# Kernel optimization log

Measured on AMD Instinct MI355X. Metric: run time of the kernel, lower is better.

## Reference

```python
import jax, jax.numpy as jnp
import numpy as np

B, T, C, H = 8, 1024, 768, 12
HD = C // H  # 64, even for RoPE
ROPE_THETA = 10000.0


def precompute_freqs_cis(dim, end, theta=ROPE_THETA):
    # [end, dim//2, 2] with (cos, sin) in last axis
    freqs = 1.0 / theta ** (jnp.arange(0, dim // 2).astype(jnp.float32) / (dim // 2))
    t = jnp.arange(end)
    f = jnp.outer(t, freqs)
    return jnp.stack([jnp.cos(f), jnp.sin(f)], axis=-1)


def apply_rope(x, fc):
    # x: [B,T,H,hd]; fc: [T,1,hd//2,2] (broadcasts over B and H)
    xr = x.reshape(*x.shape[:-1], -1, 2)
    x_re, x_im = xr[..., 0], xr[..., 1]
    cos, sin = fc[..., 0], fc[..., 1]
    out_re = x_re * cos - x_im * sin
    out_im = x_re * sin + x_im * cos
    return jnp.stack([out_re, out_im], axis=-1).reshape(x.shape)


def setup_inputs() -> dict:
    key = jax.random.key(0)
    k0, k1, k2 = jax.random.split(key, 3)
    x = jax.random.normal(k0, (B, T, C), jnp.float32)
    Wqkv = jax.random.normal(k1, (C, 3 * C), jnp.float32) * 0.02
    bqkv = jnp.zeros((3 * C,), jnp.float32)
    Wproj = jax.random.normal(k2, (C, C), jnp.float32) * 0.02
    bproj = jnp.zeros((C,), jnp.float32)
    mask = jnp.tril(jnp.ones((T, T), jnp.int32))  # causal
    return {"x": x, "Wqkv": Wqkv, "bqkv": bqkv, "Wproj": Wproj, "bproj": bproj, "mask": mask}


def reference(x, Wqkv, bqkv, Wproj, bproj, mask):
    B_, T_, C_ = x.shape
    qkv = (x @ Wqkv + bqkv).reshape(B_, T_, 3, H, HD)
    q, k, v = qkv[:, :, 0], qkv[:, :, 1], qkv[:, :, 2]  # each [B,T,H,hd]
    fc = precompute_freqs_cis(HD, T_)[:, None]  # [T,1,hd//2,2]
    q = apply_rope(q, fc)
    k = apply_rope(k, fc)
    scale = 1.0 / jnp.sqrt(jnp.float32(HD))
    attn = jnp.einsum('bthd,bkhd->bhtk', q, k) * scale  # [B,H,T,T]
    neg = jnp.finfo(attn.dtype).min
    attn = jnp.where(mask[None, None, :, :] == 0, neg, attn)
    attn = jax.nn.softmax(attn, axis=-1)
    out = jnp.einsum('bhtk,bkhd->bthd', attn, v).reshape(B_, T_, C_)
    return out @ Wproj + bproj
```

## Files before the change

kernel.cpp:

```cpp
#include <hip/hip_runtime.h>
#include <cstdint>
#include <cstddef>

#define BB 8
#define TT 1024
#define CC 768
#define NH 12
#define HD 64

using bf16x8 = __attribute__((ext_vector_type(8))) short;
using f32x4  = __attribute__((ext_vector_type(4))) float;

static __device__ __forceinline__ short f2bf(float f) {
    uint32_t u;
    __builtin_memcpy(&u, &f, 4);
    u += 0x7FFFu + ((u >> 16) & 1u);
    return (short)(u >> 16);
}

static __device__ __forceinline__ uint32_t bfpack(float lo, float hi) {
    return (uint32_t)(uint16_t)f2bf(lo) | ((uint32_t)(uint16_t)f2bf(hi) << 16);
}

#define GLOAD_LDS16(gp, lp)                                                        \
    __builtin_amdgcn_global_load_lds(                                              \
        (const __attribute__((address_space(1))) void*)(gp),                       \
        (__attribute__((address_space(3))) void*)(lp), 16, 0, 0)

__global__ void fc_kernel(float2* __restrict__ fc) {
    int idx = blockIdx.x * 256 + threadIdx.x;
    int t = idx >> 5, p = idx & 31;
    float freq = powf(10000.0f, -(float)p / 32.0f);
    float a = (float)t * freq;
    fc[idx] = make_float2(cosf(a), sinf(a));
}

__global__ __launch_bounds__(256)
void cast_kernel(const float* __restrict__ in, short* __restrict__ out) {
    int i = (blockIdx.x * 256 + threadIdx.x) * 8;
    float4 f0 = *(const float4*)(in + i);
    float4 f1 = *(const float4*)(in + i + 4);
    bf16x8 h;
    h[0] = f2bf(f0.x); h[1] = f2bf(f0.y); h[2] = f2bf(f0.z); h[3] = f2bf(f0.w);
    h[4] = f2bf(f1.x); h[5] = f2bf(f1.y); h[6] = f2bf(f1.z); h[7] = f2bf(f1.w);
    *(bf16x8*)(out + i) = h;
}

__global__ __launch_bounds__(256)
void transpose_cast_kernel(const float* __restrict__ in, short* __restrict__ out,
                           int R, int Cdim) {
    __shared__ float tile[32][33];
    int tx = threadIdx.x, ty = threadIdx.y;
    int c0 = blockIdx.x * 32, r0 = blockIdx.y * 32;
#pragma unroll
    for (int i = 0; i < 4; i++)
        tile[ty + 8 * i][tx] = in[(size_t)(r0 + ty + 8 * i) * Cdim + c0 + tx];
    __syncthreads();
#pragma unroll
    for (int i = 0; i < 4; i++)
        out[(size_t)(c0 + ty + 8 * i) * R + r0 + tx] = f2bf(tile[tx][ty + 8 * i]);
}

__global__ __launch_bounds__(256)
void vtrans_kernel(const short* __restrict__ V, short* __restrict__ VT) {
    __shared__ short tl[64][72];
    const int tid = threadIdx.x;
    const int bh = blockIdx.y, t0 = blockIdx.x * 64;
    {
        int r = tid >> 2, cs = (tid & 3) * 16;
        const short* src = V + (size_t)bh * TT * HD + (size_t)(t0 + r) * HD + cs;
        *(bf16x8*)&tl[r][cs]     = *(const bf16x8*)src;
        *(bf16x8*)&tl[r][cs + 8] = *(const bf16x8*)(src + 8);
    }
    __syncthreads();
    {
        int d = tid >> 2, ts = (tid & 3) * 16;
        bf16x8 o0, o1;
#pragma unroll
        for (int e = 0; e < 8; e++) { o0[e] = tl[ts + e][d]; o1[e] = tl[ts + 8 + e][d]; }
        short* dst = VT + (size_t)bh * TT * HD + (size_t)d * TT + t0 + ts;
        *(bf16x8*)dst       = o0;
        *(bf16x8*)(dst + 8) = o1;
    }
}

template <int EPI>
__global__ __launch_bounds__(256)
void gemm_kernel(const short* __restrict__ Agl, const short* __restrict__ BT,
                 const float* __restrict__ bias,
                 short* __restrict__ Qb, short* __restrict__ Kb, short* __restrict__ Vb,
                 const float2* __restrict__ fc, float* __restrict__ out) {
    __shared__ __align__(16) char smem[65536];
    const int tid = threadIdx.x;
    const int lane = tid & 63, wid = tid >> 6;
    const int g = lane >> 4, c = lane & 15;
    const int wm = wid >> 1, wn = wid & 1;

    const int nx = gridDim.x;
    const int bid = blockIdx.y * nx + blockIdx.x;
    const int cpx = (nx * gridDim.y) >> 3;
    const int swz = (bid & 7) * cpx + (bid >> 3);
    const int m0 = (swz / nx) * 128, n0 = (swz % nx) * 128;

    const int sr = lane >> 2;
    const int scol = (((lane & 3) ^ ((sr >> 1) & 3)) << 3);
    const short* Abase = Agl + (size_t)(m0 + wid * 32 + sr) * 768 + scol;
    const short* Bbase = BT  + (size_t)(n0 + wid * 32 + sr) * 768 + scol;

#define A_SLOT(b, kh, q) (smem + (b) * 32768 + (kh) * 8192 + wid * 2048 + (q) * 1024)
#define B_SLOT(b, kh, q) (smem + (b) * 32768 + 16384 + (kh) * 8192 + wid * 2048 + (q) * 1024)
#define STAGE(b, kh, kt)                                                   \
    {                                                                      \
        size_t ko = (size_t)(kt) * 64 + (kh) * 32;                         \
        GLOAD_LDS16(Abase + ko, A_SLOT(b, kh, 0));                         \
        GLOAD_LDS16(Abase + 16 * 768 + ko, A_SLOT(b, kh, 1));              \
        GLOAD_LDS16(Bbase + ko, B_SLOT(b, kh, 0));                         \
        GLOAD_LDS16(Bbase + 16 * 768 + ko, B_SLOT(b, kh, 1));              \
    }

    const f32x4 zero4 = {0.f, 0.f, 0.f, 0.f};
    f32x4 acc[4][4];
#pragma unroll
    for (int i = 0; i < 4; i++)
#pragma unroll
        for (int j = 0; j < 4; j++) acc[i][j] = zero4;

    STAGE(0, 0, 0);
    STAGE(0, 1, 0);
    STAGE(1, 0, 1);
    asm volatile("s_waitcnt vmcnt(8)" ::: "memory");
    __builtin_amdgcn_s_barrier();

    for (int t = 0; t < 12; t++) {
        const int buf = t & 1;
        const int t1 = (t + 1 < 12) ? t + 1 : t - 11;
        const int t2 = (t + 2 < 12) ? t + 2 : t - 10;
#pragma unroll
        for (int kk = 0; kk < 2; kk++) {
            const short* Ab = (const short*)(smem + buf * 32768 + kk * 8192);
            const short* Bb = (const short*)(smem + buf * 32768 + 16384 + kk * 8192);
            bf16x8 af[4], bfr[4];
#pragma unroll
            for (int mi = 0; mi < 4; mi++) {
                int row = wm * 64 + mi * 16 + c;
                af[mi] = *(const bf16x8*)&Ab[row * 32 + ((g ^ ((row >> 1) & 3)) << 3)];
            }
#pragma unroll
            for (int ni = 0; ni < 4; ni++) {
                int row = wn * 64 + ni * 16 + c;
                bfr[ni] = *(const bf16x8*)&Bb[row * 32 + ((g ^ ((row >> 1) & 3)) << 3)];
            }
            if (kk == 0) STAGE(buf ^ 1, 1, t1)
            else         STAGE(buf, 0, t2)
            __builtin_amdgcn_s_barrier();
            __builtin_amdgcn_s_setprio(1);
#pragma unroll
            for (int mi = 0; mi < 4; mi++)
#pragma unroll
                for (int ni = 0; ni < 4; ni++)
                    acc[mi][ni] = __builtin_amdgcn_mfma_f32_16x16x32_bf16(
                        af[mi], bfr[ni], acc[mi][ni], 0, 0, 0);
            __builtin_amdgcn_s_setprio(0);
            asm volatile("s_waitcnt vmcnt(8)" ::: "memory");
            __builtin_amdgcn_s_barrier();
        }
    }

    asm volatile("s_waitcnt vmcnt(0)" ::: "memory");
    __builtin_amdgcn_s_barrier();

    if (EPI == 0) {
        uint32_t* LD = (uint32_t*)smem;
#pragma unroll
        for (int ni = 0; ni < 4; ni++) {
            int nl = wn * 64 + ni * 16 + c;
            int n = n0 + nl;
            float bv = bias[n];
            int part = (n >= 1536) ? 2 : (n >= 768 ? 1 : 0);
            int d = (n - part * 768) & 63;
#pragma unroll
            for (int mi = 0; mi < 4; mi++) {
#pragma unroll
                for (int r = 0; r < 4; r++) {
                    int ml = wm * 64 + mi * 16 + g * 4 + r;
                    float v = acc[mi][ni][r] + bv;
                    float pv = __shfl_xor(v, 1);
                    if (!(c & 1)) {
                        float o0, o1;
                        if (part < 2) {
                            int t = (m0 + ml) & 1023;
                            float2 cs = fc[t * 32 + (d >> 1)];
                            o0 = v * cs.x - pv * cs.y;
                            o1 = v * cs.y + pv * cs.x;
                            if (part == 0) { o0 *= 0.125f; o1 *= 0.125f; }
                        } else { o0 = v; o1 = pv; }
                        LD[ml * 64 + ((nl >> 1) ^ (((ml >> 2) & 3) << 3))] = bfpack(o0, o1);
                    }
                }
            }
        }
        __syncthreads();
#pragma unroll
        for (int p = 0; p < 8; p++) {
            int ml = p * 16 + (tid >> 4);
            int wc = (tid & 15) * 4;
            int4 dat = *(const int4*)&LD[ml * 64 + (wc ^ (((ml >> 2) & 3) << 3))];
            int n = n0 + wc * 2;
            int part = (n >= 1536) ? 2 : (n >= 768 ? 1 : 0);
            int rem = n - part * 768;
            int h = rem >> 6, d = rem & 63;
            int m = m0 + ml, b = m >> 10, t = m & 1023;
            short* dst = (part == 0 ? Qb : part == 1 ? Kb : Vb)
                         + (((size_t)b * NH + h) * TT + t) * HD + d;
            *(int4*)dst = dat;
        }
    } else {
#pragma unroll
        for (int mi = 0; mi < 4; mi++)
#pragma unroll
            for (int ni = 0; ni < 4; ni++) {
                int n = n0 + wn * 64 + ni * 16 + c;
                float bv = bias[n];
#pragma unroll
                for (int r = 0; r < 4; r++) {
                    int m = m0 + wm * 64 + mi * 16 + g * 4 + r;
                    out[(size_t)m * CC + n] = acc[mi][ni][r] + bv;
                }
            }
    }
#undef A_SLOT
#undef B_SLOT
#undef STAGE
}

__global__ __launch_bounds__(256)
void attn_kernel(const short* __restrict__ Qb, const short* __restrict__ Kb,
                 const short* __restrict__ VT, short* __restrict__ Ob) {
    __shared__ uint32_t Pt[4][32][32];
    __shared__ uint32_t ot[128 * 32];
    const int tid = threadIdx.x, lane = tid & 63, wid = tid >> 6;
    const int g = lane >> 4, c = lane & 15;
    const int bh = blockIdx.x, qb = 7 - (int)blockIdx.y;
    const int b = bh / NH, h = bh % NH;
    const short* Qp = Qb + (size_t)bh * TT * HD;
    const short* Kp = Kb + (size_t)bh * TT * HD;
    const short* Vp = VT + (size_t)bh * TT * HD;
    const int q0 = qb * 128 + wid * 32;
    const int sw = (c & 7) << 2;

    bf16x8 qf[2][2];
#pragma unroll
    for (int qs = 0; qs < 2; qs++)
#pragma unroll
        for (int kh = 0; kh < 2; kh++)
            qf[qs][kh] = *(const bf16x8*)(Qp + (size_t)(q0 + qs * 16 + c) * HD + kh * 32 + g * 8);

    const f32x4 zero4 = {0.f, 0.f, 0.f, 0.f};
    f32x4 o[2][4];
#pragma unroll
    for (int qs = 0; qs < 2; qs++)
#pragma unroll
        for (int dt = 0; dt < 4; dt++) o[qs][dt] = zero4;
    float mrun[2] = {-1e30f, -1e30f}, lrun[2] = {0.f, 0.f};

    const int t0max = ((q0 + 31) >> 6) << 6;
    for (int t0 = 0; t0 <= t0max; t0 += 64) {
        f32x4 st[2][4];
#pragma unroll
        for (int nt = 0; nt < 4; nt++) {
            const short* kp = Kp + (size_t)(t0 + nt * 16 + c) * HD + g * 8;
            bf16x8 k0 = *(const bf16x8*)kp;
            bf16x8 k1 = *(const bf16x8*)(kp + 32);
#pragma unroll
            for (int qs = 0; qs < 2; qs++) {
                f32x4 z = zero4;
                z = __builtin_amdgcn_mfma_f32_16x16x32_bf16(k0, qf[qs][0], z, 0, 0, 0);
                z = __builtin_amdgcn_mfma_f32_16x16x32_bf16(k1, qf[qs][1], z, 0, 0, 0);
                st[qs][nt] = z;
            }
        }
        bf16x8 vf[2][4];
#pragma unroll
        for (int blk = 0; blk < 2; blk++)
#pragma unroll
            for (int dt = 0; dt < 4; dt++)
                vf[blk][dt] = *(const bf16x8*)(Vp + (size_t)(dt * 16 + c) * TT + t0 + blk * 32 + g * 8);
        if (t0 + 63 > q0) {
#pragma unroll
            for (int qs = 0; qs < 2; qs++) {
                int q = q0 + qs * 16 + c;
#pragma unroll
                for (int nt = 0; nt < 4; nt++)
#pragma unroll
                    for (int r = 0; r < 4; r++)
                        if (t0 + nt * 16 + g * 4 + r > q) st[qs][nt][r] = -1e30f;
            }
        }
#pragma unroll
        for (int qs = 0; qs < 2; qs++) {
            float mx = st[qs][0][0];
#pragma unroll
            for (int nt = 0; nt < 4; nt++)
#pragma unroll
                for (int r = 0; r < 4; r++) mx = fmaxf(mx, st[qs][nt][r]);
            mx = fmaxf(mx, __shfl_xor(mx, 16));
            mx = fmaxf(mx, __shfl_xor(mx, 32));
            float mnew = fmaxf(mrun[qs], mx);
            float al = __expf(mrun[qs] - mnew);
            mrun[qs] = mnew;
            float sm = 0.f;
#pragma unroll
            for (int nt = 0; nt < 4; nt++)
#pragma unroll
                for (int r = 0; r < 4; r++) {
                    float e = __expf(st[qs][nt][r] - mnew);
                    st[qs][nt][r] = e;
                    sm += e;
                }
            sm += __shfl_xor(sm, 16);
            sm += __shfl_xor(sm, 32);
            lrun[qs] = lrun[qs] * al + sm;
#pragma unroll
            for (int dt = 0; dt < 4; dt++) {
                o[qs][dt][0] *= al; o[qs][dt][1] *= al;
                o[qs][dt][2] *= al; o[qs][dt][3] *= al;
            }
            int row = qs * 16 + c;
#pragma unroll
            for (int nt = 0; nt < 4; nt++) {
                uint32_t w0 = bfpack(st[qs][nt][0], st[qs][nt][1]);
                uint32_t w1 = bfpack(st[qs][nt][2], st[qs][nt][3]);
                int wa = nt * 8 + 2 * g;
                Pt[wid][row][wa ^ sw]       = w0;
                Pt[wid][row][(wa + 1) ^ sw] = w1;
            }
        }
#pragma unroll
        for (int qs = 0; qs < 2; qs++) {
            int row = qs * 16 + c;
#pragma unroll
            for (int blk = 0; blk < 2; blk++) {
                bf16x8 pf = *(const bf16x8*)&Pt[wid][row][(blk * 16 + 4 * g) ^ sw];
#pragma unroll
                for (int dt = 0; dt < 4; dt++)
                    o[qs][dt] = __builtin_amdgcn_mfma_f32_16x16x32_bf16(
                        vf[blk][dt], pf, o[qs][dt], 0, 0, 0);
            }
        }
    }

#pragma unroll
    for (int qs = 0; qs < 2; qs++) {
        float inv = 1.0f / lrun[qs];
        int ql = wid * 32 + qs * 16 + c;
#pragma unroll
        for (int dt = 0; dt < 4; dt++) {
            uint32_t w0 = bfpack(o[qs][dt][0] * inv, o[qs][dt][1] * inv);
            uint32_t w1 = bfpack(o[qs][dt][2] * inv, o[qs][dt][3] * inv);
            int jc0 = dt * 8 + 2 * g;
            int jc1 = jc0 + 1;
            ot[ql * 32 + ((((jc0 >> 2) ^ (c & 7)) << 2) | (jc0 & 3))] = w0;
            ot[ql * 32 + ((((jc1 >> 2) ^ (c & 7)) << 2) | (jc1 & 3))] = w1;
        }
    }
    __syncthreads();
#pragma unroll
    for (int p = 0; p < 4; p++) {
        int q = (tid >> 3) + 32 * p;
        int jb = tid & 7;
        const uint32_t* src = &ot[q * 32 + ((jb ^ (q & 7)) << 2)];
        int4 w = *(const int4*)src;
        *(int4*)(Ob + ((size_t)b * TT + qb * 128 + q) * CC + h * HD + jb * 8) = w;
    }
}

extern "C" void kernel_launch(void* const* d_in, const int* in_sizes, int n_in,
                              void* d_out, int out_size, void* d_ws, size_t ws_size,
                              hipStream_t stream) {
    const float* x     = (const float*)d_in[0];
    const float* Wqkv  = (const float*)d_in[1];
    const float* bqkv  = (const float*)d_in[2];
    const float* Wproj = (const float*)d_in[3];
    const float* bproj = (const float*)d_in[4];

    char* ws = (char*)d_ws;
    short*  WqkvT  = (short*)(ws);
    short*  WprojT = (short*)(ws + 3538944);
    float2* fc     = (float2*)(ws + 3538944 + 1179648);
    short*  Qb     = (short*)(ws + 4980736);
    short*  Kb     = (short*)(ws + 4980736 + 1 * 12582912);
    short*  VOb    = (short*)(ws + 4980736 + 2 * 12582912);
    short*  VbT    = (short*)(ws + 4980736 + 3 * 12582912);
    short*  xb     = VbT;
    float*  out    = (float*)d_out;

    hipLaunchKernelGGL(fc_kernel, dim3(128), dim3(256), 0, stream, fc);
    hipLaunchKernelGGL(transpose_cast_kernel, dim3(72, 24), dim3(32, 8), 0, stream,
                       Wqkv, WqkvT, 768, 2304);
    hipLaunchKernelGGL(transpose_cast_kernel, dim3(24, 24), dim3(32, 8), 0, stream,
                       Wproj, WprojT, 768, 768);
    hipLaunchKernelGGL(cast_kernel, dim3(3072), dim3(256), 0, stream, x, xb);
    hipLaunchKernelGGL((gemm_kernel<0>), dim3(18, 64), dim3(256), 0, stream,
                       xb, WqkvT, bqkv, Qb, Kb, VOb, fc, (float*)nullptr);
    hipLaunchKernelGGL(vtrans_kernel, dim3(16, 96), dim3(256), 0, stream, VOb, VbT);
    hipLaunchKernelGGL(attn_kernel, dim3(96, 8), dim3(256), 0, stream, Qb, Kb, VbT, VOb);
    hipLaunchKernelGGL((gemm_kernel<1>), dim3(6, 64), dim3(256), 0, stream,
                       VOb, WprojT, bproj,
                       (short*)nullptr, (short*)nullptr, (short*)nullptr,
                       (const float2*)nullptr, out);
}
```

Before: 169.3 us.

## Switch GEMM K-loop to a three-slot LDS ring with one barrier per step

The GEMM main loop previously used two 32 KB buffers, each holding two 32-wide K halves, with two barriers per half-step. It now uses a three-slot ring of 16 KB slots, each holding one 32-wide K chunk. Each step prefetches the chunk two ahead into the slot read in the previous step, so the barrier between the fragment reads and the prefetch issue is dropped. This cuts barrier count and shrinks shared memory from 64 KB to 48 KB, which may allow more resident blocks. In exchange, prefetch is only two chunks deep, so global load latency may be less well hidden.

```diff
diff --git a/kernel.cpp b/kernel.cpp
--- a/kernel.cpp
+++ b/kernel.cpp
@@ -90,7 +90,7 @@
                  const float* __restrict__ bias,
                  short* __restrict__ Qb, short* __restrict__ Kb, short* __restrict__ Vb,
                  const float2* __restrict__ fc, float* __restrict__ out) {
-    __shared__ __align__(16) char smem[65536];
+    __shared__ __align__(16) char smem[49152];
     const int tid = threadIdx.x;
     const int lane = tid & 63, wid = tid >> 6;
     const int g = lane >> 4, c = lane & 15;
@@ -107,15 +107,13 @@
     const short* Abase = Agl + (size_t)(m0 + wid * 32 + sr) * 768 + scol;
     const short* Bbase = BT  + (size_t)(n0 + wid * 32 + sr) * 768 + scol;
 
-#define A_SLOT(b, kh, q) (smem + (b) * 32768 + (kh) * 8192 + wid * 2048 + (q) * 1024)
-#define B_SLOT(b, kh, q) (smem + (b) * 32768 + 16384 + (kh) * 8192 + wid * 2048 + (q) * 1024)
-#define STAGE(b, kh, kt)                                                   \
-    {                                                                      \
-        size_t ko = (size_t)(kt) * 64 + (kh) * 32;                         \
-        GLOAD_LDS16(Abase + ko, A_SLOT(b, kh, 0));                         \
-        GLOAD_LDS16(Abase + 16 * 768 + ko, A_SLOT(b, kh, 1));              \
-        GLOAD_LDS16(Bbase + ko, B_SLOT(b, kh, 0));                         \
-        GLOAD_LDS16(Bbase + 16 * 768 + ko, B_SLOT(b, kh, 1));              \
+#define STAGE(S, T, KH)                                                          \
+    {                                                                            \
+        size_t ko = (size_t)(T) * 64 + (KH) * 32;                                \
+        GLOAD_LDS16(Abase + ko,            smem + (S) * 16384 + wid * 2048);     \
+        GLOAD_LDS16(Abase + 16 * 768 + ko, smem + (S) * 16384 + wid * 2048 + 1024); \
+        GLOAD_LDS16(Bbase + ko,            smem + (S) * 16384 + 8192 + wid * 2048); \
+        GLOAD_LDS16(Bbase + 16 * 768 + ko, smem + (S) * 16384 + 8192 + wid * 2048 + 1024); \
     }
 
     const f32x4 zero4 = {0.f, 0.f, 0.f, 0.f};
@@ -126,19 +124,22 @@
         for (int j = 0; j < 4; j++) acc[i][j] = zero4;
 
     STAGE(0, 0, 0);
-    STAGE(0, 1, 0);
     STAGE(1, 0, 1);
-    asm volatile("s_waitcnt vmcnt(8)" ::: "memory");
-    __builtin_amdgcn_s_barrier();
-
-    for (int t = 0; t < 12; t++) {
-        const int buf = t & 1;
-        const int t1 = (t + 1 < 12) ? t + 1 : t - 11;
-        const int t2 = (t + 2 < 12) ? t + 2 : t - 10;
-#pragma unroll
-        for (int kk = 0; kk < 2; kk++) {
-            const short* Ab = (const short*)(smem + buf * 32768 + kk * 8192);
-            const short* Bb = (const short*)(smem + buf * 32768 + 16384 + kk * 8192);
+    asm volatile("s_waitcnt vmcnt(4)" ::: "memory");
+    asm volatile("s_barrier" ::: "memory");
+
+    for (int t3 = 0; t3 < 12; t3 += 3) {
+#pragma unroll
+        for (int pp = 0; pp < 6; pp++) {
+            const int slotR = pp % 3;
+            const int slotS = (pp + 2) % 3;
+            const int tile = t3 + (pp >> 1);
+            const int kk = pp & 1;
+            int tileS = tile + 1;
+            if (tileS >= 12) tileS -= 12;
+
+            const short* Ab = (const short*)(smem + slotR * 16384);
+            const short* Bb = (const short*)(smem + slotR * 16384 + 8192);
             bf16x8 af[4], bfr[4];
 #pragma unroll
             for (int mi = 0; mi < 4; mi++) {
@@ -150,9 +151,7 @@
                 int row = wn * 64 + ni * 16 + c;
                 bfr[ni] = *(const bf16x8*)&Bb[row * 32 + ((g ^ ((row >> 1) & 3)) << 3)];
             }
-            if (kk == 0) STAGE(buf ^ 1, 1, t1)
-            else         STAGE(buf, 0, t2)
-            __builtin_amdgcn_s_barrier();
+            STAGE(slotS, tileS, kk);
             __builtin_amdgcn_s_setprio(1);
 #pragma unroll
             for (int mi = 0; mi < 4; mi++)
@@ -161,13 +160,13 @@
                     acc[mi][ni] = __builtin_amdgcn_mfma_f32_16x16x32_bf16(
                         af[mi], bfr[ni], acc[mi][ni], 0, 0, 0);
             __builtin_amdgcn_s_setprio(0);
-            asm volatile("s_waitcnt vmcnt(8)" ::: "memory");
-            __builtin_amdgcn_s_barrier();
+            asm volatile("s_waitcnt vmcnt(4)" ::: "memory");
+            asm volatile("s_barrier" ::: "memory");
         }
     }
 
     asm volatile("s_waitcnt vmcnt(0)" ::: "memory");
-    __builtin_amdgcn_s_barrier();
+    asm volatile("s_barrier" ::: "memory");
 
     if (EPI == 0) {
         uint32_t* LD = (uint32_t*)smem;
@@ -228,8 +227,6 @@
                 }
             }
     }
-#undef A_SLOT
-#undef B_SLOT
 #undef STAGE
 }
 
```

Result: no change. 170.0 us (+0.4%).
